# Kernel optimization log

Hardware: AMD Instinct MI355X
Metric: run time of the kernel (lower is better)

The kernel has to match this reference:

```python
import jax, jax.numpy as jnp
import numpy as np

NUM_REGIONS = 20
EMBED_DIM = 768
PATCH = (4, 16, 16)          # (pd, ph, pw)
IMG = (64, 512, 512)         # (D, H, W)
B = 2
N_PATCHES = 16384


def setup_inputs() -> dict:
    key = jax.random.key(0)
    k1, k2, k3 = jax.random.split(key, 3)
    segmentation_mask = jax.random.randint(
        k1, (B, 1) + IMG, 0, NUM_REGIONS + 1, dtype=jnp.int32)
    patch_coords = jax.random.uniform(k2, (B, N_PATCHES, 3), dtype=jnp.float32)
    region_prototypes = 0.02 * jax.random.normal(
        k3, (NUM_REGIONS, EMBED_DIM), dtype=jnp.float32)
    return {"segmentation_mask": segmentation_mask,
            "patch_coords": patch_coords,
            "region_prototypes": region_prototypes}


def _compute_assignments(segmentation_mask, patch_coords):
    Bsz, _, D, H, W = segmentation_mask.shape
    pd, ph, pw = PATCH
    dims = jnp.array([D, H, W], dtype=jnp.float32)
    half = jnp.array([pd // 2, ph // 2, pw // 2], dtype=jnp.float32)

    cpix = patch_coords * dims                                   # (B,N,3)
    # torch: z_start = max(0, int(c - half)); z_end = min(D, int(c + half))
    start = jnp.maximum(0.0, jnp.floor(cpix - half)).astype(jnp.int32)   # (B,N,3)
    end = jnp.minimum(dims, jnp.floor(cpix + half)).astype(jnp.int32)    # (B,N,3)

    # per-axis index grids of fixed size, validity mask honors clipped box
    zi = start[..., 0:1] + jnp.arange(pd, dtype=jnp.int32)        # (B,N,pd)
    yi = start[..., 1:2] + jnp.arange(ph, dtype=jnp.int32)        # (B,N,ph)
    xi = start[..., 2:3] + jnp.arange(pw, dtype=jnp.int32)        # (B,N,pw)
    vz = zi < end[..., 0:1]
    vy = yi < end[..., 1:2]
    vx = xi < end[..., 2:3]

    ziC = jnp.clip(zi, 0, D - 1)
    yiC = jnp.clip(yi, 0, H - 1)
    xiC = jnp.clip(xi, 0, W - 1)

    # flattened gather: (B, N, pd, ph, pw) voxel values
    lin = (ziC[:, :, :, None, None] * (H * W)
           + yiC[:, :, None, :, None] * W
           + xiC[:, :, None, None, :])
    flat = segmentation_mask.reshape(Bsz, D * H * W)
    vals = jnp.take_along_axis(flat, lin.reshape(Bsz, -1), axis=1)
    vals = vals.reshape(Bsz, lin.shape[1], pd, ph, pw)
    valid = (vz[:, :, :, None, None]
             & vy[:, :, None, :, None]
             & vx[:, :, None, None, :])

    # numel of each (possibly clipped) crop
    extents = jnp.maximum(end - start, 0)                         # (B,N,3)
    numel = jnp.prod(extents, axis=-1).astype(jnp.float32)        # (B,N)

    # per-region counts; small fixed loop over 20 regions keeps memory low
    counts = jnp.stack(
        [jnp.sum((vals == r) & valid, axis=(2, 3, 4)).astype(jnp.float32)
         for r in range(1, NUM_REGIONS + 1)], axis=-1)            # (B,N,R)

    prop = counts / jnp.maximum(numel, 1.0)[..., None]            # zero crops -> 0
    a = prop + 1e-6
    a = a / jnp.sum(a, axis=-1, keepdims=True)
    return a


def reference(segmentation_mask, patch_coords, region_prototypes):
    Bsz = segmentation_mask.shape[0]
    region_features = jnp.broadcast_to(
        region_prototypes[None], (Bsz,) + region_prototypes.shape)
    patch_to_region = _compute_assignments(segmentation_mask, patch_coords)
    return region_features, patch_to_region
```

## Files before the change

kernel.cpp:

```cpp
#include <hip/hip_runtime.h>

#define NREG   20
#define EDIM   768
#define DVOL   64
#define HVOL   512
#define WVOL   512
#define HW_    (HVOL * WVOL)
#define DHW_   (DVOL * HVOL * WVOL)
#define NPATCH 16384
#define BTOT   2
#define PROTO_N (NREG * EDIM)
#define RF_N    (BTOT * PROTO_N)
#define TOTAL_PATCHES (BTOT * NPATCH)

struct __attribute__((packed, aligned(4))) int4p { int x, y, z, w; };

__global__ __launch_bounds__(256) void assign_kernel(
    const int*   __restrict__ seg,
    const float* __restrict__ coords,
    const float* __restrict__ proto,
    float*       __restrict__ out)
{
    __shared__ float smem[4][NREG];

    if (blockIdx.x < RF_N / 256) {
        const int i = blockIdx.x * 256 + threadIdx.x;
        out[i] = proto[i >= PROTO_N ? i - PROTO_N : i];
    }

    const int lane  = threadIdx.x & 63;
    const int wave  = threadIdx.x >> 6;
    const int patch = blockIdx.x * 4 + wave;
    const int b     = patch >> 14;

    const float c0 = coords[patch * 3 + 0] * 64.0f;
    const float c1 = coords[patch * 3 + 1] * 512.0f;
    const float c2 = coords[patch * 3 + 2] * 512.0f;

    const int sz = (int)fmaxf(0.0f,   floorf(c0 - 2.0f));
    const int ez = (int)fminf(64.0f,  floorf(c0 + 2.0f));
    const int sy = (int)fmaxf(0.0f,   floorf(c1 - 8.0f));
    const int ey = (int)fminf(512.0f, floorf(c1 + 8.0f));
    const int sx = (int)fmaxf(0.0f,   floorf(c2 - 8.0f));
    const int ex = (int)fminf(512.0f, floorf(c2 + 8.0f));

    const int xl4  = lane & 3;
    const int yy   = lane >> 2;
    const int p_lo = sx + 4 * xl4;
    const int st   = min(p_lo, WVOL - 4);
    const int yi   = sy + yy;
    const int vy   = (yi < ey) ? 1 : 0;
    const int yiC  = min(yi, HVOL - 1);
    const int base = b * DHW_;

    int vm[4];
#pragma unroll
    for (int j = 0; j < 4; ++j) {
        const int pos = st + j;
        vm[j] = (pos >= p_lo && pos < ex && vy) ? 1 : 0;
    }

    unsigned int cc[5] = {0u, 0u, 0u, 0u, 0u};

#pragma unroll
    for (int z = 0; z < 4; ++z) {
        const int zi = sz + z;
        if (zi < ez) {
            const int ziC = min(zi, DVOL - 1);
            const int4p q4 = *(const int4p*)(seg + base + ziC * HW_ + yiC * WVOL + st);
            const int vals[4] = {q4.x, q4.y, q4.z, q4.w};
#pragma unroll
            for (int j = 0; j < 4; ++j) {
                const int v = vm[j] ? vals[j] : 0;
                const int t = v - 1;
                const unsigned int inc = 1u << ((t & 3) << 3);
                const int q = t >> 2;
#pragma unroll
                for (int k = 0; k < 5; ++k)
                    cc[k] += (q == k) ? inc : 0u;
            }
        }
    }

#pragma unroll
    for (int off = 1; off < 8; off <<= 1) {
#pragma unroll
        for (int k = 0; k < 5; ++k)
            cc[k] += (unsigned int)__shfl_xor((int)cc[k], off);
    }

    unsigned int lo[5], hi[5];
#pragma unroll
    for (int k = 0; k < 5; ++k) {
        lo[k] = cc[k] & 0x00FF00FFu;
        hi[k] = (cc[k] >> 8) & 0x00FF00FFu;
    }
#pragma unroll
    for (int off = 8; off < 64; off <<= 1) {
#pragma unroll
        for (int k = 0; k < 5; ++k) {
            lo[k] += (unsigned int)__shfl_xor((int)lo[k], off);
            hi[k] += (unsigned int)__shfl_xor((int)hi[k], off);
        }
    }

    unsigned int tot = 0u;
#pragma unroll
    for (int k = 0; k < 5; ++k)
        tot += (lo[k] & 0xFFFFu) + (lo[k] >> 16) + (hi[k] & 0xFFFFu) + (hi[k] >> 16);

    if (lane == 0) {
#pragma unroll
        for (int k = 0; k < 5; ++k) {
            smem[wave][4 * k + 0] = (float)(lo[k] & 0xFFFFu);
            smem[wave][4 * k + 1] = (float)(hi[k] & 0xFFFFu);
            smem[wave][4 * k + 2] = (float)(lo[k] >> 16);
            smem[wave][4 * k + 3] = (float)(hi[k] >> 16);
        }
    }
    __syncthreads();

    const float nz = (float)max(ez - sz, 0);
    const float ny = (float)max(ey - sy, 0);
    const float nx = (float)max(ex - sx, 0);
    const float numel = nz * ny * nx;
    const float denom = fmaxf(numel, 1.0f);
    const float s = (float)tot / denom + (float)NREG * 1e-6f;

    if (lane < NREG) {
        const float cnt = smem[wave][lane];
        const float a = cnt / denom + 1e-6f;
        out[RF_N + patch * NREG + lane] = a / s;
    }
}

extern "C" void kernel_launch(void* const* d_in, const int* in_sizes, int n_in,
                              void* d_out, int out_size, void* d_ws, size_t ws_size,
                              hipStream_t stream)
{
    const int*   seg    = (const int*)d_in[0];
    const float* coords = (const float*)d_in[1];
    const float* proto  = (const float*)d_in[2];
    float*       out    = (float*)d_out;

    hipLaunchKernelGGL(assign_kernel, dim3(TOTAL_PATCHES / 4), dim3(256), 0, stream,
                       seg, coords, proto, out);
}
```

Before: 58.72 us.

## Process four patches per wave with batched loads and shuffle-based result extraction

Each wave now handles four patches instead of one. It loads their coordinates with vector float4 reads and issues all sixteen row gathers up front, so memory latency overlaps across patches. The z-validity branch is replaced by bitmasks, and the shared-memory staging plus __syncthreads is replaced by per-lane selection of packed counts. The grid is a quarter of its former size, which raises register use and may lower occupancy or parallelism.

```diff
diff --git a/kernel.cpp b/kernel.cpp
--- a/kernel.cpp
+++ b/kernel.cpp
@@ -12,6 +12,7 @@
 #define PROTO_N (NREG * EDIM)
 #define RF_N    (BTOT * PROTO_N)
 #define TOTAL_PATCHES (BTOT * NPATCH)
+#define PPW     4
 
 struct __attribute__((packed, aligned(4))) int4p { int x, y, z, w; };
 
@@ -21,116 +22,134 @@
     const float* __restrict__ proto,
     float*       __restrict__ out)
 {
-    __shared__ float smem[4][NREG];
-
     if (blockIdx.x < RF_N / 256) {
         const int i = blockIdx.x * 256 + threadIdx.x;
         out[i] = proto[i >= PROTO_N ? i - PROTO_N : i];
     }
 
-    const int lane  = threadIdx.x & 63;
-    const int wave  = threadIdx.x >> 6;
-    const int patch = blockIdx.x * 4 + wave;
-    const int b     = patch >> 14;
+    const int lane = threadIdx.x & 63;
+    const int gw   = blockIdx.x * 4 + (threadIdx.x >> 6);
+    const int p0   = gw * PPW;
+    const int segbase = (p0 >> 14) * DHW_;
 
-    const float c0 = coords[patch * 3 + 0] * 64.0f;
-    const float c1 = coords[patch * 3 + 1] * 512.0f;
-    const float c2 = coords[patch * 3 + 2] * 512.0f;
+    const int xl4 = lane & 3;
+    const int yy  = lane >> 2;
 
-    const int sz = (int)fmaxf(0.0f,   floorf(c0 - 2.0f));
-    const int ez = (int)fminf(64.0f,  floorf(c0 + 2.0f));
-    const int sy = (int)fmaxf(0.0f,   floorf(c1 - 8.0f));
-    const int ey = (int)fminf(512.0f, floorf(c1 + 8.0f));
-    const int sx = (int)fmaxf(0.0f,   floorf(c2 - 8.0f));
-    const int ex = (int)fminf(512.0f, floorf(c2 + 8.0f));
-
-    const int xl4  = lane & 3;
-    const int yy   = lane >> 2;
-    const int p_lo = sx + 4 * xl4;
-    const int st   = min(p_lo, WVOL - 4);
-    const int yi   = sy + yy;
-    const int vy   = (yi < ey) ? 1 : 0;
-    const int yiC  = min(yi, HVOL - 1);
-    const int base = b * DHW_;
-
-    int vm[4];
-#pragma unroll
-    for (int j = 0; j < 4; ++j) {
-        const int pos = st + j;
-        vm[j] = (pos >= p_lo && pos < ex && vy) ? 1 : 0;
+    float c[12];
+    {
+        const float4* cp = (const float4*)(coords + p0 * 3);
+        const float4 a = cp[0], bq = cp[1], d = cp[2];
+        c[0]=a.x; c[1]=a.y; c[2]=a.z; c[3]=a.w;
+        c[4]=bq.x; c[5]=bq.y; c[6]=bq.z; c[7]=bq.w;
+        c[8]=d.x; c[9]=d.y; c[10]=d.z; c[11]=d.w;
     }
 
-    unsigned int cc[5] = {0u, 0u, 0u, 0u, 0u};
+    int4p    q[PPW][4];
+    unsigned vm[PPW][4];
+    unsigned zbits[PPW];
+    float    denomv[PPW];
 
 #pragma unroll
-    for (int z = 0; z < 4; ++z) {
-        const int zi = sz + z;
-        if (zi < ez) {
-            const int ziC = min(zi, DVOL - 1);
-            const int4p q4 = *(const int4p*)(seg + base + ziC * HW_ + yiC * WVOL + st);
-            const int vals[4] = {q4.x, q4.y, q4.z, q4.w};
+    for (int p = 0; p < PPW; ++p) {
+        const float c0 = c[3*p + 0] * 64.0f;
+        const float c1 = c[3*p + 1] * 512.0f;
+        const float c2 = c[3*p + 2] * 512.0f;
+
+        const int sz = (int)fmaxf(0.0f,   floorf(c0 - 2.0f));
+        const int ez = (int)fminf(64.0f,  floorf(c0 + 2.0f));
+        const int sy = (int)fmaxf(0.0f,   floorf(c1 - 8.0f));
+        const int ey = (int)fminf(512.0f, floorf(c1 + 8.0f));
+        const int sx = (int)fmaxf(0.0f,   floorf(c2 - 8.0f));
+        const int ex = (int)fminf(512.0f, floorf(c2 + 8.0f));
+
+        const int p_lo = sx + 4 * xl4;
+        const int st   = min(p_lo, WVOL - 4);
+        const int yi   = sy + yy;
+        const unsigned vy = (yi < ey) ? 0xFFFFFFFFu : 0u;
+        const int yiC  = min(yi, HVOL - 1);
+        const int rowbase = segbase + yiC * WVOL + st;
+
 #pragma unroll
-            for (int j = 0; j < 4; ++j) {
-                const int v = vm[j] ? vals[j] : 0;
-                const int t = v - 1;
-                const unsigned int inc = 1u << ((t & 3) << 3);
-                const int q = t >> 2;
+        for (int j = 0; j < 4; ++j) {
+            const int pos = st + j;
+            vm[p][j] = (pos >= p_lo && pos < ex) ? vy : 0u;
+        }
+        unsigned zb = 0u;
 #pragma unroll
-                for (int k = 0; k < 5; ++k)
-                    cc[k] += (q == k) ? inc : 0u;
-            }
+        for (int z = 0; z < 4; ++z) {
+            zb |= (sz + z < ez) ? (1u << z) : 0u;
+            const int ziC = min(sz + z, DVOL - 1);
+            q[p][z] = *(const int4p*)(seg + rowbase + ziC * HW_);
         }
+        zbits[p] = zb;
+
+        const float nz = (float)max(ez - sz, 0);
+        const float ny = (float)max(ey - sy, 0);
+        const float nx = (float)max(ex - sx, 0);
+        denomv[p] = fmaxf(nz * ny * nx, 1.0f);
     }
 
 #pragma unroll
-    for (int off = 1; off < 8; off <<= 1) {
+    for (int p = 0; p < PPW; ++p) {
+        unsigned cc[5] = {0u, 0u, 0u, 0u, 0u};
+
 #pragma unroll
-        for (int k = 0; k < 5; ++k)
-            cc[k] += (unsigned int)__shfl_xor((int)cc[k], off);
-    }
+        for (int z = 0; z < 4; ++z) {
+            const unsigned zm = 0u - ((zbits[p] >> z) & 1u);
+            const int vals[4] = {q[p][z].x, q[p][z].y, q[p][z].z, q[p][z].w};
+#pragma unroll
+            for (int j = 0; j < 4; ++j) {
+                const int v = vals[j] & (int)(vm[p][j] & zm);
+                const int t = v - 1;
+                const unsigned inc = 1u << ((t & 3) << 3);
+                const int qk = t >> 2;
+#pragma unroll
+                for (int k = 0; k < 5; ++k)
+                    cc[k] += (qk == k) ? inc : 0u;
+            }
+        }
 
-    unsigned int lo[5], hi[5];
 #pragma unroll
-    for (int k = 0; k < 5; ++k) {
-        lo[k] = cc[k] & 0x00FF00FFu;
-        hi[k] = (cc[k] >> 8) & 0x00FF00FFu;
-    }
+        for (int off = 1; off < 8; off <<= 1) {
 #pragma unroll
-    for (int off = 8; off < 64; off <<= 1) {
+            for (int k = 0; k < 5; ++k)
+                cc[k] += (unsigned)__shfl_xor((int)cc[k], off);
+        }
+
+        unsigned lo[5], hi[5];
 #pragma unroll
         for (int k = 0; k < 5; ++k) {
-            lo[k] += (unsigned int)__shfl_xor((int)lo[k], off);
-            hi[k] += (unsigned int)__shfl_xor((int)hi[k], off);
+            lo[k] = cc[k] & 0x00FF00FFu;
+            hi[k] = (cc[k] >> 8) & 0x00FF00FFu;
         }
-    }
+#pragma unroll
+        for (int off = 8; off < 64; off <<= 1) {
+#pragma unroll
+            for (int k = 0; k < 5; ++k) {
+                lo[k] += (unsigned)__shfl_xor((int)lo[k], off);
+                hi[k] += (unsigned)__shfl_xor((int)hi[k], off);
+            }
+        }
 
-    unsigned int tot = 0u;
+        unsigned S = 0u;
 #pragma unroll
-    for (int k = 0; k < 5; ++k)
-        tot += (lo[k] & 0xFFFFu) + (lo[k] >> 16) + (hi[k] & 0xFFFFu) + (hi[k] >> 16);
+        for (int k = 0; k < 5; ++k) S += lo[k] + hi[k];
+        const unsigned tot = (S & 0xFFFFu) + (S >> 16);
 
-    if (lane == 0) {
-#pragma unroll
-        for (int k = 0; k < 5; ++k) {
-            smem[wave][4 * k + 0] = (float)(lo[k] & 0xFFFFu);
-            smem[wave][4 * k + 1] = (float)(hi[k] & 0xFFFFu);
-            smem[wave][4 * k + 2] = (float)(lo[k] >> 16);
-            smem[wave][4 * k + 3] = (float)(hi[k] >> 16);
+        const int r = lane & 3;
+        const unsigned sLo = (lane < 4) ? lo[0] : (lane < 8) ? lo[1]
+                           : (lane < 12) ? lo[2] : (lane < 16) ? lo[3] : lo[4];
+        const unsigned sHi = (lane < 4) ? hi[0] : (lane < 8) ? hi[1]
+                           : (lane < 12) ? hi[2] : (lane < 16) ? hi[3] : hi[4];
+        const unsigned fld = (r & 1) ? sHi : sLo;
+        const unsigned cnt = (r & 2) ? (fld >> 16) : (fld & 0xFFFFu);
+
+        if (lane < NREG) {
+            const float denom = denomv[p];
+            const float s = (float)tot / denom + (float)NREG * 1e-6f;
+            const float a = (float)cnt / denom + 1e-6f;
+            out[RF_N + (p0 + p) * NREG + lane] = a / s;
         }
-    }
-    __syncthreads();
-
-    const float nz = (float)max(ez - sz, 0);
-    const float ny = (float)max(ey - sy, 0);
-    const float nx = (float)max(ex - sx, 0);
-    const float numel = nz * ny * nx;
-    const float denom = fmaxf(numel, 1.0f);
-    const float s = (float)tot / denom + (float)NREG * 1e-6f;
-
-    if (lane < NREG) {
-        const float cnt = smem[wave][lane];
-        const float a = cnt / denom + 1e-6f;
-        out[RF_N + patch * NREG + lane] = a / s;
     }
 }
 
@@ -143,6 +162,6 @@
     const float* proto  = (const float*)d_in[2];
     float*       out    = (float*)d_out;
 
-    hipLaunchKernelGGL(assign_kernel, dim3(TOTAL_PATCHES / 4), dim3(256), 0, stream,
-                       seg, coords, proto, out);
+    hipLaunchKernelGGL(assign_kernel, dim3(TOTAL_PATCHES / (PPW * 4)), dim3(256),
+                       0, stream, seg, coords, proto, out);
 }
```

After: 62.54 us. 6.5% more time.
